# Kernel tuning notes

Hardware: AMD Instinct MI355X
Metric: run time of the kernel (lower is better)

## Reference

```python
import jax, jax.numpy as jnp
import numpy as np
from jax import lax

B, S, CIN, COUT, K = 32, 2048, 256, 256, 16


def setup_inputs() -> dict:
    key = jax.random.key(0)
    k1, k2, k3, k4 = jax.random.split(key, 4)
    x = jax.random.normal(k1, (B, S, CIN), dtype=jnp.float32)
    w_real = jax.random.normal(k2, (COUT, CIN, K), dtype=jnp.float32) * 0.1
    w_imag = jax.random.normal(k3, (COUT, CIN, K), dtype=jnp.float32) * 0.1
    phases = jax.random.normal(k4, (K,), dtype=jnp.float32) * 0.1
    return {"x": x, "w_real": w_real, "w_imag": w_imag, "phases": phases}


def reference(x, w_real, w_imag, phases):
    # out[b,t,o] = Re( sum_{k,i} x[b,t+k,i] * exp(1j*phases[k]) * (w_real + 1j*w_imag)[o,i,k] )
    # x is real, so this equals a real valid conv1d with effective kernel:
    #   w_eff[o,i,k] = cos(phases[k]) * w_real[o,i,k] - sin(phases[k]) * w_imag[o,i,k]
    w_eff = jnp.cos(phases)[None, None, :] * w_real - jnp.sin(phases)[None, None, :] * w_imag
    # conv expects NCH / OIH layouts
    y = lax.conv_general_dilated(
        jnp.transpose(x, (0, 2, 1)),  # [B, CIN, S]
        w_eff,                         # [COUT, CIN, K]
        window_strides=(1,),
        padding="VALID",
        dimension_numbers=("NCH", "OIH", "NCH"),
    )
    return jnp.transpose(y, (0, 2, 1))  # [B, S-K+1, COUT]
```

## Files before the change

kernel.cpp:

```cpp
#include <hip/hip_runtime.h>
#include <math.h>

#define B_    32
#define S_    2048
#define CIN_  256
#define COUT_ 256
#define K_    16
#define TOUT_ 2033
#define RTOT_ 4096

typedef __bf16 bf16x4 __attribute__((ext_vector_type(4)));
typedef __bf16 bf16x8 __attribute__((ext_vector_type(8)));
typedef float  f32x4  __attribute__((ext_vector_type(4)));

#define GLOBAL_AS __attribute__((address_space(1)))
#define LDS_AS    __attribute__((address_space(3)))

__device__ __forceinline__ void gload_lds16(const void* g, void* l) {
  __builtin_amdgcn_global_load_lds((const GLOBAL_AS void*)g, (LDS_AS void*)l, 16, 0, 0);
}

__global__ void __launch_bounds__(256) build_wt_kernel(const float* __restrict__ wr,
                                                       const float* __restrict__ wi,
                                                       const float* __restrict__ ph,
                                                       __bf16* __restrict__ wt) {
  int t = blockIdx.x * 256 + threadIdx.x;
  int o = t >> 8, i = t & 255;
  const float4* wr4 = (const float4*)(wr + (size_t)(o * CIN_ + i) * K_);
  const float4* wi4 = (const float4*)(wi + (size_t)(o * CIN_ + i) * K_);
  float re[16], im[16];
  #pragma unroll
  for (int v = 0; v < 4; v++) {
    float4 a = wr4[v];
    re[4*v+0]=a.x; re[4*v+1]=a.y; re[4*v+2]=a.z; re[4*v+3]=a.w;
    float4 b = wi4[v];
    im[4*v+0]=b.x; im[4*v+1]=b.y; im[4*v+2]=b.z; im[4*v+3]=b.w;
  }
  #pragma unroll
  for (int kk = 0; kk < K_; kk++) {
    float p = ph[kk];
    wt[(size_t)o * RTOT_ + kk * CIN_ + i] = (__bf16)(cosf(p)*re[kk] - sinf(p)*im[kk]);
  }
}

__global__ void __launch_bounds__(256, 3) conv_mfma_kernel(const float* __restrict__ xg,
                                                           const __bf16* __restrict__ wt,
                                                           float* __restrict__ out) {
  __shared__ __align__(16) __bf16 As[144 * 32];
  __shared__ __align__(16) __bf16 Bs[4][128 * 32];

  const int bx = blockIdx.x;
  const int nb = bx & 1;
  const int mb = (bx >> 1) & 15;
  const int b  = bx >> 5;

  const int tid  = threadIdx.x;
  const int w    = tid >> 6;
  const int lane = tid & 63;
  const int wm   = w >> 1, wn = w & 1;
  const int n16  = lane & 15, q = lane >> 4;

  const int t0 = mb * 128;
  const int o0 = nb * 128;

  const float* xbase = xg + (size_t)b * (S_ * CIN_);

  const int sr = tid >> 3;
  const int sc = (tid & 7) * 4;
  const int br = w * 16 + (lane >> 2);
  const int bc = (lane & 3) * 8;

  f32x4 acc[4][4];
  #pragma unroll
  for (int im_ = 0; im_ < 4; im_++)
    #pragma unroll
    for (int in_ = 0; in_ < 4; in_++)
      acc[im_][in_] = {0.f, 0.f, 0.f, 0.f};

  auto stage_a = [&](int ic) {
    const float* xcol = xbase + ic * 32 + sc;
    #pragma unroll
    for (int p = 0; p < 4; p++) {
      int r = p * 32 + sr;
      int rg = t0 + r; rg = (rg < S_) ? rg : (S_ - 1);
      float4 v = *(const float4*)(xcol + (size_t)rg * CIN_);
      bf16x4 o4; o4[0]=(__bf16)v.x; o4[1]=(__bf16)v.y; o4[2]=(__bf16)v.z; o4[3]=(__bf16)v.w;
      *(bf16x4*)(As + r * 32 + sc) = o4;
    }
    if (tid < 128) {
      int r = 128 + sr;
      int rg = t0 + r; rg = (rg < S_) ? rg : (S_ - 1);
      float4 v = *(const float4*)(xcol + (size_t)rg * CIN_);
      bf16x4 o4; o4[0]=(__bf16)v.x; o4[1]=(__bf16)v.y; o4[2]=(__bf16)v.z; o4[3]=(__bf16)v.w;
      *(bf16x4*)(As + r * 32 + sc) = o4;
    }
  };

  auto stage_b = [&](int j) {
    const int kk = j & 15;
    const int i0 = (j >> 4) * 32;
    const __bf16* wcol = wt + (size_t)kk * CIN_ + i0 + bc;
    __bf16* dst = &Bs[j & 3][(w * 16) * 32];
    #pragma unroll
    for (int p = 0; p < 2; p++) {
      int orow = o0 + p * 64 + br;
      gload_lds16(wcol + (size_t)orow * RTOT_, (void*)(dst + p * 64 * 32));
    }
  };

  stage_a(0);
  stage_b(0);
  stage_b(1);
  asm volatile("s_waitcnt vmcnt(2) lgkmcnt(0)\n\ts_barrier" ::: "memory");

  for (int j = 0; j < 128; ++j) {
    if (j + 2 < 128) stage_b(j + 2);

    const int kk = j & 15;
    const __bf16* bsr = Bs[j & 3];
    bf16x8 af[4], bfrag[4];
    #pragma unroll
    for (int jm = 0; jm < 4; jm++) {
      int row = kk + wm * 64 + jm * 16 + n16;
      af[jm] = *(const bf16x8*)(As + row * 32 + q * 8);
    }
    #pragma unroll
    for (int jn = 0; jn < 4; jn++) {
      int row = wn * 64 + jn * 16 + n16;
      bfrag[jn] = *(const bf16x8*)(bsr + row * 32 + q * 8);
    }

    __builtin_amdgcn_s_setprio(1);
    #pragma unroll
    for (int jm = 0; jm < 4; jm++)
      #pragma unroll
      for (int jn = 0; jn < 4; jn++)
        acc[jm][jn] = __builtin_amdgcn_mfma_f32_16x16x32_bf16(af[jm], bfrag[jn], acc[jm][jn], 0, 0, 0);
    __builtin_amdgcn_s_setprio(0);

    if (j == 127) break;

    if (j <= 125) asm volatile("s_waitcnt vmcnt(2)\n\ts_barrier" ::: "memory");
    else          asm volatile("s_waitcnt vmcnt(0)\n\ts_barrier" ::: "memory");

    if ((kk == 15)) {
      stage_a((j + 1) >> 4);
      asm volatile("s_waitcnt lgkmcnt(0)\n\ts_barrier" ::: "memory");
    }
  }

  float* obase = out + (size_t)b * TOUT_ * COUT_;
  #pragma unroll
  for (int jm = 0; jm < 4; jm++) {
    #pragma unroll
    for (int r = 0; r < 4; r++) {
      int t = t0 + wm * 64 + jm * 16 + q * 4 + r;
      if (t < TOUT_) {
        float* orow = obase + (size_t)t * COUT_ + o0 + wn * 64 + n16;
        #pragma unroll
        for (int jn = 0; jn < 4; jn++)
          orow[jn * 16] = acc[jm][jn][r];
      }
    }
  }
}

extern "C" void kernel_launch(void* const* d_in, const int* in_sizes, int n_in,
                              void* d_out, int out_size, void* d_ws, size_t ws_size,
                              hipStream_t stream) {
  const float* x  = (const float*)d_in[0];
  const float* wr = (const float*)d_in[1];
  const float* wi = (const float*)d_in[2];
  const float* ph = (const float*)d_in[3];
  float* out = (float*)d_out;

  __bf16* wt = (__bf16*)d_ws;

  build_wt_kernel<<<dim3((COUT_ * CIN_) / 256), dim3(256), 0, stream>>>(wr, wi, ph, wt);
  conv_mfma_kernel<<<dim3(B_ * 16 * 2), dim3(256), 0, stream>>>(x, wt, out);
}
```

Before: 270.0 us.

## Prefetch activation tiles into registers early and raise occupancy with triple-buffered weights

Splits activation staging into an early global-to-register load, issued two iterations before the tile is needed, and a later convert-and-store to LDS. This hides global load latency behind the MFMA loop. It also cuts the weight ring buffer from four stages to three, with explicit read and write indices, so four blocks per CU fit in LDS, and raises the launch-bounds occupancy hint to match. The risks are that the extra prefetch registers on top of the 64 accumulator registers hit the tighter VGPR budget of 4 blocks per CU and cause spills, and that the shallower buffer ring reduces slack.

```diff
diff --git a/kernel.cpp b/kernel.cpp
--- a/kernel.cpp
+++ b/kernel.cpp
@@ -43,11 +43,11 @@
   }
 }
 
-__global__ void __launch_bounds__(256, 3) conv_mfma_kernel(const float* __restrict__ xg,
+__global__ void __launch_bounds__(256, 4) conv_mfma_kernel(const float* __restrict__ xg,
                                                            const __bf16* __restrict__ wt,
                                                            float* __restrict__ out) {
   __shared__ __align__(16) __bf16 As[144 * 32];
-  __shared__ __align__(16) __bf16 Bs[4][128 * 32];
+  __shared__ __align__(16) __bf16 Bs[3][128 * 32];
 
   const int bx = blockIdx.x;
   const int nb = bx & 1;
@@ -77,30 +77,43 @@
     for (int in_ = 0; in_ < 4; in_++)
       acc[im_][in_] = {0.f, 0.f, 0.f, 0.f};
 
-  auto stage_a = [&](int ic) {
+  float4 a_pref[5];
+
+  auto issue_a = [&](int ic) {
     const float* xcol = xbase + ic * 32 + sc;
     #pragma unroll
     for (int p = 0; p < 4; p++) {
       int r = p * 32 + sr;
       int rg = t0 + r; rg = (rg < S_) ? rg : (S_ - 1);
-      float4 v = *(const float4*)(xcol + (size_t)rg * CIN_);
-      bf16x4 o4; o4[0]=(__bf16)v.x; o4[1]=(__bf16)v.y; o4[2]=(__bf16)v.z; o4[3]=(__bf16)v.w;
-      *(bf16x4*)(As + r * 32 + sc) = o4;
+      a_pref[p] = *(const float4*)(xcol + (size_t)rg * CIN_);
     }
     if (tid < 128) {
       int r = 128 + sr;
       int rg = t0 + r; rg = (rg < S_) ? rg : (S_ - 1);
-      float4 v = *(const float4*)(xcol + (size_t)rg * CIN_);
+      a_pref[4] = *(const float4*)(xcol + (size_t)rg * CIN_);
+    }
+  };
+  auto commit_a = [&]() {
+    #pragma unroll
+    for (int p = 0; p < 4; p++) {
+      int r = p * 32 + sr;
+      float4 v = a_pref[p];
       bf16x4 o4; o4[0]=(__bf16)v.x; o4[1]=(__bf16)v.y; o4[2]=(__bf16)v.z; o4[3]=(__bf16)v.w;
       *(bf16x4*)(As + r * 32 + sc) = o4;
     }
+    if (tid < 128) {
+      int r = 128 + sr;
+      float4 v = a_pref[4];
+      bf16x4 o4; o4[0]=(__bf16)v.x; o4[1]=(__bf16)v.y; o4[2]=(__bf16)v.z; o4[3]=(__bf16)v.w;
+      *(bf16x4*)(As + r * 32 + sc) = o4;
+    }
   };
 
-  auto stage_b = [&](int j) {
+  auto stage_b = [&](int j, int buf) {
     const int kk = j & 15;
     const int i0 = (j >> 4) * 32;
     const __bf16* wcol = wt + (size_t)kk * CIN_ + i0 + bc;
-    __bf16* dst = &Bs[j & 3][(w * 16) * 32];
+    __bf16* dst = &Bs[0][0] + buf * (128 * 32) + (w * 16) * 32;
     #pragma unroll
     for (int p = 0; p < 2; p++) {
       int orow = o0 + p * 64 + br;
@@ -108,16 +121,22 @@
     }
   };
 
-  stage_a(0);
-  stage_b(0);
-  stage_b(1);
+  issue_a(0);
+  commit_a();
+  stage_b(0, 0);
+  stage_b(1, 1);
   asm volatile("s_waitcnt vmcnt(2) lgkmcnt(0)\n\ts_barrier" ::: "memory");
 
+  int jr = 0;
+  int jw = 2;
+  #pragma unroll 1
   for (int j = 0; j < 128; ++j) {
-    if (j + 2 < 128) stage_b(j + 2);
-
     const int kk = j & 15;
-    const __bf16* bsr = Bs[j & 3];
+
+    if (kk == 14 && j != 126) issue_a((j >> 4) + 1);
+    if (j + 2 < 128) stage_b(j + 2, jw);
+
+    const __bf16* bsr = &Bs[0][0] + jr * (128 * 32);
     bf16x8 af[4], bfrag[4];
     #pragma unroll
     for (int jm = 0; jm < 4; jm++) {
@@ -143,10 +162,13 @@
     if (j <= 125) asm volatile("s_waitcnt vmcnt(2)\n\ts_barrier" ::: "memory");
     else          asm volatile("s_waitcnt vmcnt(0)\n\ts_barrier" ::: "memory");
 
-    if ((kk == 15)) {
-      stage_a((j + 1) >> 4);
+    if (kk == 15) {
+      commit_a();
       asm volatile("s_waitcnt lgkmcnt(0)\n\ts_barrier" ::: "memory");
     }
+
+    jr = (jr == 2) ? 0 : jr + 1;
+    jw = (jw == 2) ? 0 : jw + 1;
   }
 
   float* obase = out + (size_t)b * TOUT_ * COUT_;
```

New measurement: 238.4 us. 11.7% less time.
